# Performance work log

Measured on AMD Instinct MI355X. Metric: run time of the kernel, lower is better.

## Reference

```python
import jax, jax.numpy as jnp
import numpy as np

NUM_EXPERTS = 64
TOP_K = 8
HIDDEN = 1024
INTER = 768
BATCH, SEQ = 1, 1024
CAPACITY = 256


def setup_inputs() -> dict:
    key = jax.random.key(0)
    k1, k2, k3, k4, k5 = jax.random.split(key, 5)
    scale = 0.02
    return {
        "hidden_states": jax.random.normal(k1, (BATCH, SEQ, HIDDEN), dtype=jnp.float32),
        "gate_w": jax.random.normal(k2, (NUM_EXPERTS, HIDDEN), dtype=jnp.float32) * scale,
        "w_gate": jax.random.normal(k3, (NUM_EXPERTS, INTER, HIDDEN), dtype=jnp.float32) * scale,
        "w_up": jax.random.normal(k4, (NUM_EXPERTS, INTER, HIDDEN), dtype=jnp.float32) * scale,
        "w_down": jax.random.normal(k5, (NUM_EXPERTS, HIDDEN, INTER), dtype=jnp.float32) * scale,
    }


def _moe_forward(hidden_states, gate_w, w_gate, w_up, w_down):
    B, S, H = hidden_states.shape
    x = hidden_states.reshape(-1, H)                      # [T, H]
    T = x.shape[0]

    # Router: linear -> float32 softmax -> top-k -> renormalize (fused in Int4MoePlugin)
    logits = (x @ gate_w.T).astype(jnp.float32)           # [T, E]
    probs = jax.nn.softmax(logits, axis=-1)
    topk_p, topk_i = jax.lax.top_k(probs, TOP_K)          # [T, K]
    topk_p = topk_p / jnp.sum(topk_p, axis=-1, keepdims=True)

    # Dispatch each (token, k) assignment into a per-expert slot (Switch-style)
    flat_e = topk_i.reshape(-1)                           # [T*K] int32
    onehot = jax.nn.one_hot(flat_e, NUM_EXPERTS, dtype=jnp.int32)
    pos_all = jnp.cumsum(onehot, axis=0) - 1              # [T*K, E]
    pos = jnp.take_along_axis(pos_all, flat_e[:, None], axis=1)[:, 0]  # [T*K]

    x_rep = jnp.repeat(x, TOP_K, axis=0)                  # [T*K, H]
    dispatch = jnp.zeros((NUM_EXPERTS, CAPACITY, H), x.dtype)
    dispatch = dispatch.at[flat_e, pos].set(x_rep, mode="drop")  # [E, C, H]

    # Grouped expert MLP: silu(x Wg^T) * (x Wu^T) then Wd^T
    g = jax.nn.silu(jnp.einsum("ech,eih->eci", dispatch, w_gate))
    u = jnp.einsum("ech,eih->eci", dispatch, w_up)
    y = jnp.einsum("eci,ehi->ech", g * u, w_down)         # [E, C, H]

    # Combine back to tokens with routing weights
    valid = (pos < CAPACITY)
    y_tok = y[flat_e, jnp.minimum(pos, CAPACITY - 1)]     # [T*K, H]
    w = (topk_p.reshape(-1) * valid.astype(topk_p.dtype)).astype(x.dtype)
    out = (y_tok * w[:, None]).reshape(T, TOP_K, H).sum(axis=1)
    return out.reshape(B, S, H)


def reference(hidden_states, gate_w, w_gate, w_up, w_down):
    return _moe_forward(hidden_states, gate_w, w_gate, w_up, w_down)
```

## Files before the change

### kernel.cpp

```cpp
#include <hip/hip_runtime.h>

#define T_TOK 1024
#define HID   1024
#define NE    64
#define TOPKK 8
#define ITR   768
#define CAP   256

typedef __attribute__((ext_vector_type(4))) float f32x4;
typedef __attribute__((ext_vector_type(8))) short s16x8;

#define OFF_COUNTS 0
#define OFF_TOPKI  1024
#define OFF_SLOT   (OFF_TOPKI + T_TOK*TOPKK*4)
#define OFF_TOPKW  (OFF_SLOT  + T_TOK*TOPKK*4)
#define OFF_ETOK   (OFF_TOPKW + T_TOK*TOPKK*4)
#define OFF_XD     (1 << 18)
#define OFF_G      (OFF_XD + (size_t)NE*CAP*HID*2)
#define OFF_Y      OFF_XD

__device__ __forceinline__ unsigned short f2bf(float f) {
  union { float f; unsigned u; } v; v.f = f;
  unsigned r = v.u + 0x7FFFu + ((v.u >> 16) & 1u);
  return (unsigned short)(r >> 16);
}
__device__ __forceinline__ float bf2f(unsigned short h) {
  union { unsigned u; float f; } v; v.u = ((unsigned)h) << 16;
  return v.f;
}
__device__ __forceinline__ unsigned pack2(float a, float b) {
  return (unsigned)f2bf(a) | ((unsigned)f2bf(b) << 16);
}

__device__ __forceinline__ void gld_lds16(const unsigned short* g, unsigned short* l) {
  __builtin_amdgcn_global_load_lds(
      (const __attribute__((address_space(1))) unsigned int*)g,
      (__attribute__((address_space(3))) unsigned int*)l, 16, 0, 0);
}

__global__ __launch_bounds__(256) void router_k(
    const float* __restrict__ x, const float* __restrict__ gw,
    int* __restrict__ topki, float* __restrict__ topkw, int* __restrict__ counts)
{
  int t = blockIdx.x, tid = threadIdx.x;
  if (t == 0 && tid < NE) counts[tid] = 0;
  __shared__ float xs[HID];
  __shared__ double parts[4 * 64];
  *(f32x4*)&xs[tid * 4] = *(const f32x4*)(x + (size_t)t * HID + tid * 4);
  __syncthreads();
  int e = tid & 63, part = tid >> 6;
  const float* g  = gw + (size_t)e * HID + part * 256;
  const float* xp = xs + part * 256;
  double acc = 0.0;
  #pragma unroll 4
  for (int h = 0; h < 256; h += 4) {
    f32x4 gv = *(const f32x4*)(g + h);
    f32x4 xv = *(const f32x4*)(xp + h);
    acc += (double)xv.x * gv.x + (double)xv.y * gv.y
         + (double)xv.z * gv.z + (double)xv.w * gv.w;
  }
  parts[part * 64 + e] = acc;
  __syncthreads();
  if (tid < 64) {
    double l = parts[tid] + parts[64 + tid] + parts[128 + tid] + parts[192 + tid];
    double m = l;
    for (int off = 32; off >= 1; off >>= 1) {
      double o = __shfl_xor(m, off, 64);
      m = o > m ? o : m;
    }
    double p  = exp(l - m);
    double pv = p;
    double wv[TOPKK]; int wi[TOPKK];
    double sum8 = 0.0;
    #pragma unroll
    for (int j = 0; j < TOPKK; ++j) {
      double bv = pv; int bi = tid;
      for (int off = 32; off >= 1; off >>= 1) {
        double ov = __shfl_xor(bv, off, 64);
        int    oi = __shfl_xor(bi, off, 64);
        if (ov > bv || (ov == bv && oi < bi)) { bv = ov; bi = oi; }
      }
      wv[j] = bv; wi[j] = bi; sum8 += bv;
      if (tid == bi) pv = -1.0;
    }
    if (tid == 0) {
      double inv = 1.0 / sum8;
      #pragma unroll
      for (int j = 0; j < TOPKK; ++j) {
        topki[t * TOPKK + j] = wi[j];
        topkw[t * TOPKK + j] = (float)(wv[j] * inv);
      }
    }
  }
}

__global__ __launch_bounds__(256) void assign_k(
    const int* __restrict__ topki, int* __restrict__ counts,
    int* __restrict__ slot_of, int* __restrict__ etok)
{
  int a = blockIdx.x * 256 + threadIdx.x;
  if (a >= T_TOK * TOPKK) return;
  int e = topki[a];
  int s = atomicAdd(counts + e, 1);
  if (s < CAP) { slot_of[a] = s; etok[e * CAP + s] = a >> 3; }
  else         { slot_of[a] = -1; }
}

__global__ __launch_bounds__(128) void dispatch_k(
    const float* __restrict__ x, const int* __restrict__ counts,
    const int* __restrict__ etok, unsigned short* __restrict__ Xd)
{
  int b = blockIdx.x;
  int e = b >> 8, s = b & 255;
  int cnt = min(counts[e], CAP);
  if (s >= cnt) return;
  int t = etok[b];
  const float* src = x + (size_t)t * HID;
  unsigned short* dst = Xd + (size_t)b * HID;
  int tid = threadIdx.x;
  #pragma unroll
  for (int i = 0; i < 2; ++i) {
    int h = (tid + i * 128) * 4;
    f32x4 v = *(const f32x4*)(src + h);
    ushort4 o;
    o.x = f2bf(v.x); o.y = f2bf(v.y); o.z = f2bf(v.z); o.w = f2bf(v.w);
    *(ushort4*)(dst + h) = o;
  }
}

__global__ __launch_bounds__(256, 2) void gemm1_k(
    const unsigned short* __restrict__ Xd, const float* __restrict__ wg,
    const float* __restrict__ wu, const int* __restrict__ counts,
    unsigned short* __restrict__ G)
{
  int bx = blockIdx.x;
  int ct = bx % 12;
  int e  = bx / 12;
  int cnt = min(counts[e], CAP);
  if (cnt <= 0) return;
  int ru = (cnt + 63) & ~63;

  __shared__ unsigned short As[CAP * 64];
  __shared__ unsigned short Bg[64 * 64];
  __shared__ unsigned short Bu[64 * 64];

  int tid = threadIdx.x;
  int lane = tid & 63, w = tid >> 6;
  bool wactive = (w * 64) < ru;

  const unsigned short* Abase = Xd + (size_t)e * CAP * HID;
  const float* gbase = wg + ((size_t)e * ITR + ct * 64) * HID;
  const float* ubase = wu + ((size_t)e * ITR + ct * 64) * HID;

  int br = tid >> 3;
  int bs = tid & 7;

  f32x4 pg[2][2], pu[2][2];
  #pragma unroll
  for (int j = 0; j < 2; ++j) {
    const float* p0 = gbase + (size_t)(br + j * 32) * HID + bs * 8;
    pg[j][0] = *(const f32x4*)p0;  pg[j][1] = *(const f32x4*)(p0 + 4);
    const float* p1 = ubase + (size_t)(br + j * 32) * HID + bs * 8;
    pu[j][0] = *(const f32x4*)p1;  pu[j][1] = *(const f32x4*)(p1 + 4);
  }

  f32x4 accg[4][4], accu[4][4];
  #pragma unroll
  for (int i = 0; i < 4; ++i)
    #pragma unroll
    for (int j = 0; j < 4; ++j) { accg[i][j] = (f32x4)0.0f; accu[i][j] = (f32x4)0.0f; }

  for (int kc = 0; kc < HID / 64; ++kc) {
    int k0 = kc * 64;
    __syncthreads();
    #pragma unroll
    for (int i = 0; i < 8; ++i) {
      if (i * 32 < ru) {
        int q = tid + i * 256;
        int r = q >> 3, s = q & 7;
        int ss = s ^ (r & 7);
        gld_lds16(Abase + (size_t)r * HID + k0 + ss * 8, &As[q * 8]);
      }
    }
    #pragma unroll
    for (int j = 0; j < 2; ++j) {
      int r = br + j * 32;
      int sw = bs ^ (r & 7);
      uint4 pk;
      pk.x = pack2(pg[j][0].x, pg[j][0].y); pk.y = pack2(pg[j][0].z, pg[j][0].w);
      pk.z = pack2(pg[j][1].x, pg[j][1].y); pk.w = pack2(pg[j][1].z, pg[j][1].w);
      *(uint4*)&Bg[r * 64 + sw * 8] = pk;
      pk.x = pack2(pu[j][0].x, pu[j][0].y); pk.y = pack2(pu[j][0].z, pu[j][0].w);
      pk.z = pack2(pu[j][1].x, pu[j][1].y); pk.w = pack2(pu[j][1].z, pu[j][1].w);
      *(uint4*)&Bu[r * 64 + sw * 8] = pk;
    }
    __syncthreads();
    if (kc + 1 < HID / 64) {
      int k1 = k0 + 64;
      #pragma unroll
      for (int j = 0; j < 2; ++j) {
        const float* p0 = gbase + (size_t)(br + j * 32) * HID + k1 + bs * 8;
        pg[j][0] = *(const f32x4*)p0;  pg[j][1] = *(const f32x4*)(p0 + 4);
        const float* p1 = ubase + (size_t)(br + j * 32) * HID + k1 + bs * 8;
        pu[j][0] = *(const f32x4*)p1;  pu[j][1] = *(const f32x4*)(p1 + 4);
      }
    }
    if (wactive) {
      #pragma unroll
      for (int ks = 0; ks < 2; ++ks) {
        int t = ks * 4 + (lane >> 4);
        s16x8 af[4];
        #pragma unroll
        for (int mt = 0; mt < 4; ++mt) {
          int R = w * 64 + mt * 16 + (lane & 15);
          af[mt] = *(const s16x8*)&As[R * 64 + (t ^ (R & 7)) * 8];
        }
        #pragma unroll
        for (int nt = 0; nt < 4; ++nt) {
          int rB = nt * 16 + (lane & 15);
          int sB = (t ^ (rB & 7)) * 8;
          s16x8 bg = *(const s16x8*)&Bg[rB * 64 + sB];
          s16x8 bu = *(const s16x8*)&Bu[rB * 64 + sB];
          #pragma unroll
          for (int mt = 0; mt < 4; ++mt) {
            accg[mt][nt] = __builtin_amdgcn_mfma_f32_16x16x32_bf16(af[mt], bg, accg[mt][nt], 0, 0, 0);
            accu[mt][nt] = __builtin_amdgcn_mfma_f32_16x16x32_bf16(af[mt], bu, accu[mt][nt], 0, 0, 0);
          }
        }
      }
    }
  }
  if (wactive) {
    unsigned short* Gout = G + (size_t)e * CAP * ITR;
    #pragma unroll
    for (int mt = 0; mt < 4; ++mt)
      #pragma unroll
      for (int nt = 0; nt < 4; ++nt)
        #pragma unroll
        for (int r = 0; r < 4; ++r) {
          int row = w * 64 + mt * 16 + (lane >> 4) * 4 + r;
          int col = ct * 64 + nt * 16 + (lane & 15);
          float gv = accg[mt][nt][r];
          float uv = accu[mt][nt][r];
          float sg = gv / (1.0f + __expf(-gv));
          Gout[(size_t)row * ITR + col] = f2bf(sg * uv);
        }
  }
}

__global__ __launch_bounds__(256, 3) void gemm2_k(
    const unsigned short* __restrict__ G, const float* __restrict__ wd,
    const int* __restrict__ counts, unsigned short* __restrict__ Y)
{
  int bx = blockIdx.x;
  int ct = bx & 15;
  int e  = bx >> 4;
  int cnt = min(counts[e], CAP);
  if (cnt <= 0) return;
  int ru = (cnt + 63) & ~63;

  __shared__ unsigned short As[CAP * 64];
  __shared__ unsigned short Bs[64 * 64];

  int tid = threadIdx.x;
  int lane = tid & 63, w = tid >> 6;
  bool wactive = (w * 64) < ru;

  const unsigned short* Abase = G + (size_t)e * CAP * ITR;
  const float* bbase = wd + ((size_t)e * HID + ct * 64) * ITR;

  int br = tid >> 3, bs = tid & 7;

  f32x4 pb[2][2];
  #pragma unroll
  for (int j = 0; j < 2; ++j) {
    const float* p0 = bbase + (size_t)(br + j * 32) * ITR + bs * 8;
    pb[j][0] = *(const f32x4*)p0;  pb[j][1] = *(const f32x4*)(p0 + 4);
  }

  f32x4 acc[4][4];
  #pragma unroll
  for (int i = 0; i < 4; ++i)
    #pragma unroll
    for (int j = 0; j < 4; ++j) acc[i][j] = (f32x4)0.0f;

  for (int kc = 0; kc < ITR / 64; ++kc) {
    int k0 = kc * 64;
    __syncthreads();
    #pragma unroll
    for (int i = 0; i < 8; ++i) {
      if (i * 32 < ru) {
        int q = tid + i * 256;
        int r = q >> 3, s = q & 7;
        int ss = s ^ (r & 7);
        gld_lds16(Abase + (size_t)r * ITR + k0 + ss * 8, &As[q * 8]);
      }
    }
    #pragma unroll
    for (int j = 0; j < 2; ++j) {
      int r = br + j * 32;
      int sw = bs ^ (r & 7);
      uint4 pk;
      pk.x = pack2(pb[j][0].x, pb[j][0].y); pk.y = pack2(pb[j][0].z, pb[j][0].w);
      pk.z = pack2(pb[j][1].x, pb[j][1].y); pk.w = pack2(pb[j][1].z, pb[j][1].w);
      *(uint4*)&Bs[r * 64 + sw * 8] = pk;
    }
    __syncthreads();
    if (kc + 1 < ITR / 64) {
      int k1 = k0 + 64;
      #pragma unroll
      for (int j = 0; j < 2; ++j) {
        const float* p0 = bbase + (size_t)(br + j * 32) * ITR + k1 + bs * 8;
        pb[j][0] = *(const f32x4*)p0;  pb[j][1] = *(const f32x4*)(p0 + 4);
      }
    }
    if (wactive) {
      #pragma unroll
      for (int ks = 0; ks < 2; ++ks) {
        int t = ks * 4 + (lane >> 4);
        s16x8 af[4];
        #pragma unroll
        for (int mt = 0; mt < 4; ++mt) {
          int R = w * 64 + mt * 16 + (lane & 15);
          af[mt] = *(const s16x8*)&As[R * 64 + (t ^ (R & 7)) * 8];
        }
        #pragma unroll
        for (int nt = 0; nt < 4; ++nt) {
          int rB = nt * 16 + (lane & 15);
          s16x8 bf = *(const s16x8*)&Bs[rB * 64 + (t ^ (rB & 7)) * 8];
          #pragma unroll
          for (int mt = 0; mt < 4; ++mt)
            acc[mt][nt] = __builtin_amdgcn_mfma_f32_16x16x32_bf16(af[mt], bf, acc[mt][nt], 0, 0, 0);
        }
      }
    }
  }
  if (wactive) {
    unsigned short* Yout = Y + (size_t)e * CAP * HID;
    #pragma unroll
    for (int mt = 0; mt < 4; ++mt)
      #pragma unroll
      for (int nt = 0; nt < 4; ++nt)
        #pragma unroll
        for (int r = 0; r < 4; ++r) {
          int row = w * 64 + mt * 16 + (lane >> 4) * 4 + r;
          int col = ct * 64 + nt * 16 + (lane & 15);
          Yout[(size_t)row * HID + col] = f2bf(acc[mt][nt][r]);
        }
  }
}

__global__ __launch_bounds__(256) void combine_k(
    const unsigned short* __restrict__ Y, const int* __restrict__ topki,
    const int* __restrict__ slot_of, const float* __restrict__ topkw,
    float* __restrict__ out)
{
  int t = blockIdx.x, tid = threadIdx.x;
  int h = tid * 4;
  float a0 = 0.f, a1 = 0.f, a2 = 0.f, a3 = 0.f;
  #pragma unroll
  for (int k = 0; k < TOPKK; ++k) {
    int a = t * TOPKK + k;
    int s = slot_of[a];
    if (s < 0) continue;
    int e = topki[a];
    float wt = topkw[a];
    const unsigned short* yp = Y + ((size_t)(e * CAP + s)) * HID + h;
    ushort4 yv = *(const ushort4*)yp;
    a0 += wt * bf2f(yv.x);
    a1 += wt * bf2f(yv.y);
    a2 += wt * bf2f(yv.z);
    a3 += wt * bf2f(yv.w);
  }
  f32x4 o = { a0, a1, a2, a3 };
  *(f32x4*)(out + (size_t)t * HID + h) = o;
}

extern "C" void kernel_launch(void* const* d_in, const int* in_sizes, int n_in,
                              void* d_out, int out_size, void* d_ws, size_t ws_size,
                              hipStream_t stream)
{
  const float* x     = (const float*)d_in[0];
  const float* gw    = (const float*)d_in[1];
  const float* wgate = (const float*)d_in[2];
  const float* wup   = (const float*)d_in[3];
  const float* wdown = (const float*)d_in[4];
  float* out = (float*)d_out;

  char* ws = (char*)d_ws;
  int*   counts  = (int*)  (ws + OFF_COUNTS);
  int*   topki   = (int*)  (ws + OFF_TOPKI);
  int*   slot_of = (int*)  (ws + OFF_SLOT);
  float* topkw   = (float*)(ws + OFF_TOPKW);
  int*   etok    = (int*)  (ws + OFF_ETOK);
  unsigned short* Xd = (unsigned short*)(ws + OFF_XD);
  unsigned short* G  = (unsigned short*)(ws + OFF_G);
  unsigned short* Y  = (unsigned short*)(ws + OFF_Y);

  router_k  <<<T_TOK, 256, 0, stream>>>(x, gw, topki, topkw, counts);
  assign_k  <<<(T_TOK * TOPKK) / 256, 256, 0, stream>>>(topki, counts, slot_of, etok);
  dispatch_k<<<NE * CAP, 128, 0, stream>>>(x, counts, etok, Xd);
  gemm1_k   <<<NE * 12, 256, 0, stream>>>(Xd, wgate, wup, counts, G);
  gemm2_k   <<<NE * 16, 256, 0, stream>>>(G, wdown, counts, Y);
  combine_k <<<T_TOK, 256, 0, stream>>>(Y, topki, slot_of, topkw, out);
}
```

Before: 612.6 us.

## Double-buffer LDS tiles and use 512-thread blocks in expert GEMMs

Both expert GEMM kernels now keep two LDS buffers for the A and B tiles and prefetch the next K-chunk while computing the current one, so only one barrier is needed per iteration. Block size doubles to 512 threads (8 waves), with each wave owning 32 rows instead of 64, which halves accumulator registers per thread. The aim is to hide global and LDS load latency behind MFMA work and raise occupancy. In exchange, LDS use doubles (about 80KB per block in gemm1), which may limit how many blocks fit on a CU.

```diff
diff --git a/kernel.cpp b/kernel.cpp
--- a/kernel.cpp
+++ b/kernel.cpp
@@ -128,7 +128,7 @@
   }
 }
 
-__global__ __launch_bounds__(256, 2) void gemm1_k(
+__global__ __launch_bounds__(512, 2) void gemm1_k(
     const unsigned short* __restrict__ Xd, const float* __restrict__ wg,
     const float* __restrict__ wu, const int* __restrict__ counts,
     unsigned short* __restrict__ G)
@@ -140,105 +140,104 @@
   if (cnt <= 0) return;
   int ru = (cnt + 63) & ~63;
 
-  __shared__ unsigned short As[CAP * 64];
-  __shared__ unsigned short Bg[64 * 64];
-  __shared__ unsigned short Bu[64 * 64];
+  __shared__ unsigned short As[2][CAP * 64];
+  __shared__ unsigned short Bg[2][64 * 64];
+  __shared__ unsigned short Bu[2][64 * 64];
 
   int tid = threadIdx.x;
   int lane = tid & 63, w = tid >> 6;
-  bool wactive = (w * 64) < ru;
+  bool wactive = (w * 32) < ru;
 
   const unsigned short* Abase = Xd + (size_t)e * CAP * HID;
   const float* gbase = wg + ((size_t)e * ITR + ct * 64) * HID;
   const float* ubase = wu + ((size_t)e * ITR + ct * 64) * HID;
 
-  int br = tid >> 3;
-  int bs = tid & 7;
-
-  f32x4 pg[2][2], pu[2][2];
-  #pragma unroll
-  for (int j = 0; j < 2; ++j) {
-    const float* p0 = gbase + (size_t)(br + j * 32) * HID + bs * 8;
-    pg[j][0] = *(const f32x4*)p0;  pg[j][1] = *(const f32x4*)(p0 + 4);
-    const float* p1 = ubase + (size_t)(br + j * 32) * HID + bs * 8;
-    pu[j][0] = *(const f32x4*)p1;  pu[j][1] = *(const f32x4*)(p1 + 4);
-  }
-
-  f32x4 accg[4][4], accu[4][4];
-  #pragma unroll
-  for (int i = 0; i < 4; ++i)
+  int br = tid >> 3, bs = tid & 7;
+  int swb = (bs ^ (br & 7)) * 8;
+  const float* gp = gbase + (size_t)br * HID + bs * 8;
+  const float* up = ubase + (size_t)br * HID + bs * 8;
+
+  #pragma unroll
+  for (int i = 0; i < 4; ++i) if (i * 64 < ru) {
+    int q = tid + i * 512;
+    int r = q >> 3, s = q & 7;
+    gld_lds16(Abase + (size_t)r * HID + (s ^ (r & 7)) * 8, &As[0][q * 8]);
+  }
+  {
+    f32x4 g0 = *(const f32x4*)gp, g1 = *(const f32x4*)(gp + 4);
+    f32x4 u0 = *(const f32x4*)up, u1 = *(const f32x4*)(up + 4);
+    uint4 pk;
+    pk.x = pack2(g0.x, g0.y); pk.y = pack2(g0.z, g0.w);
+    pk.z = pack2(g1.x, g1.y); pk.w = pack2(g1.z, g1.w);
+    *(uint4*)&Bg[0][br * 64 + swb] = pk;
+    pk.x = pack2(u0.x, u0.y); pk.y = pack2(u0.z, u0.w);
+    pk.z = pack2(u1.x, u1.y); pk.w = pack2(u1.z, u1.w);
+    *(uint4*)&Bu[0][br * 64 + swb] = pk;
+  }
+  __syncthreads();
+
+  f32x4 accg[2][4], accu[2][4];
+  #pragma unroll
+  for (int i = 0; i < 2; ++i)
     #pragma unroll
     for (int j = 0; j < 4; ++j) { accg[i][j] = (f32x4)0.0f; accu[i][j] = (f32x4)0.0f; }
 
   for (int kc = 0; kc < HID / 64; ++kc) {
-    int k0 = kc * 64;
-    __syncthreads();
-    #pragma unroll
-    for (int i = 0; i < 8; ++i) {
-      if (i * 32 < ru) {
-        int q = tid + i * 256;
+    int cur = kc & 1, nxt = cur ^ 1;
+    int k1 = (kc + 1) * 64;
+    bool more = (kc + 1 < HID / 64);
+    f32x4 g0, g1, u0, u1;
+    if (more) {
+      #pragma unroll
+      for (int i = 0; i < 4; ++i) if (i * 64 < ru) {
+        int q = tid + i * 512;
         int r = q >> 3, s = q & 7;
-        int ss = s ^ (r & 7);
-        gld_lds16(Abase + (size_t)r * HID + k0 + ss * 8, &As[q * 8]);
-      }
-    }
-    #pragma unroll
-    for (int j = 0; j < 2; ++j) {
-      int r = br + j * 32;
-      int sw = bs ^ (r & 7);
-      uint4 pk;
-      pk.x = pack2(pg[j][0].x, pg[j][0].y); pk.y = pack2(pg[j][0].z, pg[j][0].w);
-      pk.z = pack2(pg[j][1].x, pg[j][1].y); pk.w = pack2(pg[j][1].z, pg[j][1].w);
-      *(uint4*)&Bg[r * 64 + sw * 8] = pk;
-      pk.x = pack2(pu[j][0].x, pu[j][0].y); pk.y = pack2(pu[j][0].z, pu[j][0].w);
-      pk.z = pack2(pu[j][1].x, pu[j][1].y); pk.w = pack2(pu[j][1].z, pu[j][1].w);
-      *(uint4*)&Bu[r * 64 + sw * 8] = pk;
-    }
-    __syncthreads();
-    if (kc + 1 < HID / 64) {
-      int k1 = k0 + 64;
-      #pragma unroll
-      for (int j = 0; j < 2; ++j) {
-        const float* p0 = gbase + (size_t)(br + j * 32) * HID + k1 + bs * 8;
-        pg[j][0] = *(const f32x4*)p0;  pg[j][1] = *(const f32x4*)(p0 + 4);
-        const float* p1 = ubase + (size_t)(br + j * 32) * HID + k1 + bs * 8;
-        pu[j][0] = *(const f32x4*)p1;  pu[j][1] = *(const f32x4*)(p1 + 4);
-      }
+        gld_lds16(Abase + (size_t)r * HID + k1 + (s ^ (r & 7)) * 8, &As[nxt][q * 8]);
+      }
+      g0 = *(const f32x4*)(gp + k1); g1 = *(const f32x4*)(gp + k1 + 4);
+      u0 = *(const f32x4*)(up + k1); u1 = *(const f32x4*)(up + k1 + 4);
     }
     if (wactive) {
       #pragma unroll
       for (int ks = 0; ks < 2; ++ks) {
         int t = ks * 4 + (lane >> 4);
-        s16x8 af[4];
-        #pragma unroll
-        for (int mt = 0; mt < 4; ++mt) {
-          int R = w * 64 + mt * 16 + (lane & 15);
-          af[mt] = *(const s16x8*)&As[R * 64 + (t ^ (R & 7)) * 8];
-        }
+        s16x8 af0, af1;
+        { int R = w * 32 + (lane & 15);      af0 = *(const s16x8*)&As[cur][R * 64 + (t ^ (R & 7)) * 8]; }
+        { int R = w * 32 + 16 + (lane & 15); af1 = *(const s16x8*)&As[cur][R * 64 + (t ^ (R & 7)) * 8]; }
         #pragma unroll
         for (int nt = 0; nt < 4; ++nt) {
           int rB = nt * 16 + (lane & 15);
           int sB = (t ^ (rB & 7)) * 8;
-          s16x8 bg = *(const s16x8*)&Bg[rB * 64 + sB];
-          s16x8 bu = *(const s16x8*)&Bu[rB * 64 + sB];
-          #pragma unroll
-          for (int mt = 0; mt < 4; ++mt) {
-            accg[mt][nt] = __builtin_amdgcn_mfma_f32_16x16x32_bf16(af[mt], bg, accg[mt][nt], 0, 0, 0);
-            accu[mt][nt] = __builtin_amdgcn_mfma_f32_16x16x32_bf16(af[mt], bu, accu[mt][nt], 0, 0, 0);
-          }
+          s16x8 bg = *(const s16x8*)&Bg[cur][rB * 64 + sB];
+          s16x8 bu = *(const s16x8*)&Bu[cur][rB * 64 + sB];
+          accg[0][nt] = __builtin_amdgcn_mfma_f32_16x16x32_bf16(af0, bg, accg[0][nt], 0, 0, 0);
+          accg[1][nt] = __builtin_amdgcn_mfma_f32_16x16x32_bf16(af1, bg, accg[1][nt], 0, 0, 0);
+          accu[0][nt] = __builtin_amdgcn_mfma_f32_16x16x32_bf16(af0, bu, accu[0][nt], 0, 0, 0);
+          accu[1][nt] = __builtin_amdgcn_mfma_f32_16x16x32_bf16(af1, bu, accu[1][nt], 0, 0, 0);
         }
       }
     }
-  }
+    if (more) {
+      uint4 pk;
+      pk.x = pack2(g0.x, g0.y); pk.y = pack2(g0.z, g0.w);
+      pk.z = pack2(g1.x, g1.y); pk.w = pack2(g1.z, g1.w);
+      *(uint4*)&Bg[nxt][br * 64 + swb] = pk;
+      pk.x = pack2(u0.x, u0.y); pk.y = pack2(u0.z, u0.w);
+      pk.z = pack2(u1.x, u1.y); pk.w = pack2(u1.z, u1.w);
+      *(uint4*)&Bu[nxt][br * 64 + swb] = pk;
+    }
+    __syncthreads();
+  }
+
   if (wactive) {
     unsigned short* Gout = G + (size_t)e * CAP * ITR;
     #pragma unroll
-    for (int mt = 0; mt < 4; ++mt)
+    for (int mt = 0; mt < 2; ++mt)
       #pragma unroll
       for (int nt = 0; nt < 4; ++nt)
         #pragma unroll
         for (int r = 0; r < 4; ++r) {
-          int row = w * 64 + mt * 16 + (lane >> 4) * 4 + r;
+          int row = w * 32 + mt * 16 + (lane >> 4) * 4 + r;
           int col = ct * 64 + nt * 16 + (lane & 15);
           float gv = accg[mt][nt][r];
           float uv = accu[mt][nt][r];
@@ -248,7 +247,7 @@
   }
 }
 
-__global__ __launch_bounds__(256, 3) void gemm2_k(
+__global__ __launch_bounds__(512, 4) void gemm2_k(
     const unsigned short* __restrict__ G, const float* __restrict__ wd,
     const int* __restrict__ counts, unsigned short* __restrict__ Y)
 {
@@ -259,91 +258,90 @@
   if (cnt <= 0) return;
   int ru = (cnt + 63) & ~63;
 
-  __shared__ unsigned short As[CAP * 64];
-  __shared__ unsigned short Bs[64 * 64];
+  __shared__ unsigned short As[2][CAP * 64];
+  __shared__ unsigned short Bs[2][64 * 64];
 
   int tid = threadIdx.x;
   int lane = tid & 63, w = tid >> 6;
-  bool wactive = (w * 64) < ru;
+  bool wactive = (w * 32) < ru;
 
   const unsigned short* Abase = G + (size_t)e * CAP * ITR;
   const float* bbase = wd + ((size_t)e * HID + ct * 64) * ITR;
 
   int br = tid >> 3, bs = tid & 7;
-
-  f32x4 pb[2][2];
-  #pragma unroll
-  for (int j = 0; j < 2; ++j) {
-    const float* p0 = bbase + (size_t)(br + j * 32) * ITR + bs * 8;
-    pb[j][0] = *(const f32x4*)p0;  pb[j][1] = *(const f32x4*)(p0 + 4);
-  }
-
-  f32x4 acc[4][4];
-  #pragma unroll
-  for (int i = 0; i < 4; ++i)
+  int swb = (bs ^ (br & 7)) * 8;
+  const float* bp = bbase + (size_t)br * ITR + bs * 8;
+
+  #pragma unroll
+  for (int i = 0; i < 4; ++i) if (i * 64 < ru) {
+    int q = tid + i * 512;
+    int r = q >> 3, s = q & 7;
+    gld_lds16(Abase + (size_t)r * ITR + (s ^ (r & 7)) * 8, &As[0][q * 8]);
+  }
+  {
+    f32x4 b0 = *(const f32x4*)bp, b1 = *(const f32x4*)(bp + 4);
+    uint4 pk;
+    pk.x = pack2(b0.x, b0.y); pk.y = pack2(b0.z, b0.w);
+    pk.z = pack2(b1.x, b1.y); pk.w = pack2(b1.z, b1.w);
+    *(uint4*)&Bs[0][br * 64 + swb] = pk;
+  }
+  __syncthreads();
+
+  f32x4 acc[2][4];
+  #pragma unroll
+  for (int i = 0; i < 2; ++i)
     #pragma unroll
     for (int j = 0; j < 4; ++j) acc[i][j] = (f32x4)0.0f;
 
   for (int kc = 0; kc < ITR / 64; ++kc) {
-    int k0 = kc * 64;
-    __syncthreads();
-    #pragma unroll
-    for (int i = 0; i < 8; ++i) {
-      if (i * 32 < ru) {
-        int q = tid + i * 256;
+    int cur = kc & 1, nxt = cur ^ 1;
+    int k1 = (kc + 1) * 64;
+    bool more = (kc + 1 < ITR / 64);
+    f32x4 b0, b1;
+    if (more) {
+      #pragma unroll
+      for (int i = 0; i < 4; ++i) if (i * 64 < ru) {
+        int q = tid + i * 512;
         int r = q >> 3, s = q & 7;
-        int ss = s ^ (r & 7);
-        gld_lds16(Abase + (size_t)r * ITR + k0 + ss * 8, &As[q * 8]);
-      }
-    }
-    #pragma unroll
-    for (int j = 0; j < 2; ++j) {
-      int r = br + j * 32;
-      int sw = bs ^ (r & 7);
-      uint4 pk;
-      pk.x = pack2(pb[j][0].x, pb[j][0].y); pk.y = pack2(pb[j][0].z, pb[j][0].w);
-      pk.z = pack2(pb[j][1].x, pb[j][1].y); pk.w = pack2(pb[j][1].z, pb[j][1].w);
-      *(uint4*)&Bs[r * 64 + sw * 8] = pk;
-    }
-    __syncthreads();
-    if (kc + 1 < ITR / 64) {
-      int k1 = k0 + 64;
-      #pragma unroll
-      for (int j = 0; j < 2; ++j) {
-        const float* p0 = bbase + (size_t)(br + j * 32) * ITR + k1 + bs * 8;
-        pb[j][0] = *(const f32x4*)p0;  pb[j][1] = *(const f32x4*)(p0 + 4);
-      }
+        gld_lds16(Abase + (size_t)r * ITR + k1 + (s ^ (r & 7)) * 8, &As[nxt][q * 8]);
+      }
+      b0 = *(const f32x4*)(bp + k1); b1 = *(const f32x4*)(bp + k1 + 4);
     }
     if (wactive) {
       #pragma unroll
       for (int ks = 0; ks < 2; ++ks) {
         int t = ks * 4 + (lane >> 4);
-        s16x8 af[4];
-        #pragma unroll
-        for (int mt = 0; mt < 4; ++mt) {
-          int R = w * 64 + mt * 16 + (lane & 15);
-          af[mt] = *(const s16x8*)&As[R * 64 + (t ^ (R & 7)) * 8];
-        }
+        s16x8 af0, af1;
+        { int R = w * 32 + (lane & 15);      af0 = *(const s16x8*)&As[cur][R * 64 + (t ^ (R & 7)) * 8]; }
+        { int R = w * 32 + 16 + (lane & 15); af1 = *(const s16x8*)&As[cur][R * 64 + (t ^ (R & 7)) * 8]; }
         #pragma unroll
         for (int nt = 0; nt < 4; ++nt) {
           int rB = nt * 16 + (lane & 15);
-          s16x8 bf = *(const s16x8*)&Bs[rB * 64 + (t ^ (rB & 7)) * 8];
-          #pragma unroll
-          for (int mt = 0; mt < 4; ++mt)
-            acc[mt][nt] = __builtin_amdgcn_mfma_f32_16x16x32_bf16(af[mt], bf, acc[mt][nt], 0, 0, 0);
+          int sB = (t ^ (rB & 7)) * 8;
+          s16x8 bf = *(const s16x8*)&Bs[cur][rB * 64 + sB];
+          acc[0][nt] = __builtin_amdgcn_mfma_f32_16x16x32_bf16(af0, bf, acc[0][nt], 0, 0, 0);
+          acc[1][nt] = __builtin_amdgcn_mfma_f32_16x16x32_bf16(af1, bf, acc[1][nt], 0, 0, 0);
         }
       }
     }
-  }
+    if (more) {
+      uint4 pk;
+      pk.x = pack2(b0.x, b0.y); pk.y = pack2(b0.z, b0.w);
+      pk.z = pack2(b1.x, b1.y); pk.w = pack2(b1.z, b1.w);
+      *(uint4*)&Bs[nxt][br * 64 + swb] = pk;
+    }
+    __syncthreads();
+  }
+
   if (wactive) {
     unsigned short* Yout = Y + (size_t)e * CAP * HID;
     #pragma unroll
-    for (int mt = 0; mt < 4; ++mt)
+    for (int mt = 0; mt < 2; ++mt)
       #pragma unroll
       for (int nt = 0; nt < 4; ++nt)
         #pragma unroll
         for (int r = 0; r < 4; ++r) {
-          int row = w * 64 + mt * 16 + (lane >> 4) * 4 + r;
+          int row = w * 32 + mt * 16 + (lane >> 4) * 4 + r;
           int col = ct * 64 + nt * 16 + (lane & 15);
           Yout[(size_t)row * HID + col] = f2bf(acc[mt][nt][r]);
         }
@@ -400,7 +398,7 @@
   router_k  <<<T_TOK, 256, 0, stream>>>(x, gw, topki, topkw, counts);
   assign_k  <<<(T_TOK * TOPKK) / 256, 256, 0, stream>>>(topki, counts, slot_of, etok);
   dispatch_k<<<NE * CAP, 128, 0, stream>>>(x, counts, etok, Xd);
-  gemm1_k   <<<NE * 12, 256, 0, stream>>>(Xd, wgate, wup, counts, G);
-  gemm2_k   <<<NE * 16, 256, 0, stream>>>(G, wdown, counts, Y);
+  gemm1_k   <<<NE * 12, 512, 0, stream>>>(Xd, wgate, wup, counts, G);
+  gemm2_k   <<<NE * 16, 512, 0, stream>>>(G, wdown, counts, Y);
   combine_k <<<T_TOK, 256, 0, stream>>>(Y, topki, slot_of, topkw, out);
 }
```

Result: no change. 614.6 us (+0.3%).
